# Kernel optimization log

Hardware: AMD Instinct MI355X
Metric: run time of the kernel (lower is better)

## Reference

```python
import jax, jax.numpy as jnp
import numpy as np

SQRT2 = 1.4142135623730951  # lrelu def_gain
LRELU_SLOPE = 0.2
EPS = 1e-8


def setup_inputs() -> dict:
    key = jax.random.key(0)
    k1, k2, k3, k4 = jax.random.split(key, 4)
    B, C_in, C_out, H, W, K, DLAT = 8, 512, 512, 32, 32, 3, 512
    x = jax.random.normal(k1, (B, C_in, H, W), dtype=jnp.float32)
    y = jax.random.normal(k2, (B, DLAT), dtype=jnp.float32)
    # init_std = 1.0 since use_wscale=True, lrmul=1
    weight = jax.random.normal(k3, (C_out, C_in, K, K), dtype=jnp.float32)
    mod_weight = jax.random.normal(k4, (C_in, DLAT), dtype=jnp.float32)
    bias = jnp.ones((C_in,), dtype=jnp.float32)
    return {"x": x, "y": y, "weight": weight, "mod_weight": mod_weight, "bias": bias}


def reference(x, y, weight, mod_weight, bias):
    B, C_in, H, W = x.shape
    C_out, _, K, _ = weight.shape
    dlat = mod_weight.shape[1]
    w_mul_mod = dlat ** (-0.5)  # EqualizedLinear wscale; conv w_mul is unused in forward
    # style: s = sqrt(2) * lrelu(y @ W_mod^T + b)
    s = y @ (mod_weight * w_mul_mod).T  # [B, C_in]
    s = jax.nn.leaky_relu(s + bias, LRELU_SLOPE) * SQRT2
    # modulate per-sample weights: [B, C_out, C_in, K, K]
    ww = weight[None] * s[:, None, :, None, None]
    # demodulate
    d = jax.lax.rsqrt(jnp.sum(ww * ww, axis=(2, 3, 4)) + EPS)  # [B, C_out]
    ww = ww * d[:, :, None, None, None]
    # fused grouped conv: groups = batch
    xg = x.reshape(1, B * C_in, H, W)
    wg = ww.reshape(B * C_out, C_in, K, K)
    out = jax.lax.conv_general_dilated(
        xg, wg, window_strides=(1, 1), padding="SAME",
        dimension_numbers=("NCHW", "OIHW", "NCHW"),
        feature_group_count=B)
    return out.reshape(B, C_out, H, W)
```

## Files before the change

### kernel.cpp

```cpp
#include <hip/hip_runtime.h>
#include <hip/hip_bf16.h>

typedef float f32x4 __attribute__((ext_vector_type(4)));
typedef short bf16x8 __attribute__((ext_vector_type(8)));

#define LRELU_SLOPE 0.2f
#define SQRT2F 1.4142135623730951f
#define MODSCALE 0.044194173824159216f

#define GLL(SRC, DST)                                                       \
  __builtin_amdgcn_global_load_lds(                                         \
      (const __attribute__((address_space(1))) unsigned int*)(SRC),         \
      (__attribute__((address_space(3))) unsigned int*)(DST), 16, 0, 0)

__global__ __launch_bounds__(256) void prep_kernel(const float* __restrict__ w,
                                                   const float* __restrict__ y,
                                                   const float* __restrict__ mw,
                                                   const float* __restrict__ bias,
                                                   __hip_bfloat16* __restrict__ wt2,
                                                   float* __restrict__ wsq,
                                                   float* __restrict__ s,
                                                   __hip_bfloat16* __restrict__ xsp) {
  const int bid = blockIdx.x;
  const int tid = threadIdx.x;
  if (bid < 1024) {
    int idx = bid * 256 + tid;
    int co = idx >> 9, ci = idx & 511;
    const float* p = w + (size_t)idx * 9;
    float v[9];
    float sq = 0.f;
#pragma unroll
    for (int t = 0; t < 9; ++t) {
      v[t] = p[t];
      sq += v[t] * v[t];
    }
    wsq[idx] = sq;
    int slabbase = ((ci >> 6) * 2 + ((ci >> 5) & 1)) * 16384 + co * 32 + (ci & 31);
#pragma unroll
    for (int t = 0; t < 9; ++t)
      wt2[t * 262144 + slabbase] = __float2bfloat16(v[t]);
  } else if (bid < 1152) {
    int l = tid & 63;
    int ci = (bid - 1024) * 4 + (tid >> 6);
    const float4* mwr = reinterpret_cast<const float4*>(mw + ci * 512);
    float4 m0 = mwr[2 * l], m1 = mwr[2 * l + 1];
    float acc[8];
#pragma unroll
    for (int b = 0; b < 8; ++b) {
      const float4* yr = reinterpret_cast<const float4*>(y + b * 512);
      float4 y0 = yr[2 * l], y1 = yr[2 * l + 1];
      acc[b] = m0.x * y0.x + m0.y * y0.y + m0.z * y0.z + m0.w * y0.w +
               m1.x * y1.x + m1.y * y1.y + m1.z * y1.z + m1.w * y1.w;
    }
#pragma unroll
    for (int off = 32; off > 0; off >>= 1) {
#pragma unroll
      for (int b = 0; b < 8; ++b) acc[b] += __shfl_xor(acc[b], off, 64);
    }
    if (l < 8) {
      float v = acc[l] * MODSCALE + bias[ci];
      v = v > 0.f ? v : LRELU_SLOPE * v;
      s[l * 512 + ci] = v * SQRT2F;
    }
  } else {
    int i = (bid - 1152) * 256 + tid;
    int b = i / 8448;
    int r = i - b * 8448;
    int pos = r >> 6;
    int cj = (r & 63) << 3;
    int hr, hc;
    if (pos < 34) { hr = 0; hc = pos; }
    else if (pos < 68) { hr = 33; hc = pos - 34; }
    else if (pos < 100) { hr = pos - 67; hc = 0; }
    else { hr = pos - 99; hc = 33; }
    unsigned off = (unsigned)((b * 34 + hr) * 34 + hc) * 512 + cj;
    int4 z = {0, 0, 0, 0};
    *reinterpret_cast<int4*>(xsp + off) = z;
  }
}

__global__ __launch_bounds__(256) void xsdem_kernel(const float* __restrict__ x,
                                                    const float* __restrict__ s,
                                                    const float* __restrict__ wsq,
                                                    __hip_bfloat16* __restrict__ xsp,
                                                    float* __restrict__ d) {
  const int bid = blockIdx.x;
  const int tid = threadIdx.x;
  if (bid < 2048) {
    int cc = bid & 7;
    int h = (bid >> 3) & 31;
    int b = bid >> 8;
    __shared__ __hip_bfloat16 tile[32][72];
    int cil = tid >> 2;
    int w0 = (tid & 3) * 8;
    int ci = cc * 64 + cil;
    const float* xp = x + (((size_t)(b * 512 + ci) * 32 + h) << 5) + w0;
    float sv = s[b * 512 + ci];
    float4 a0 = *reinterpret_cast<const float4*>(xp);
    float4 a1 = *reinterpret_cast<const float4*>(xp + 4);
    tile[w0 + 0][cil] = __float2bfloat16(a0.x * sv);
    tile[w0 + 1][cil] = __float2bfloat16(a0.y * sv);
    tile[w0 + 2][cil] = __float2bfloat16(a0.z * sv);
    tile[w0 + 3][cil] = __float2bfloat16(a0.w * sv);
    tile[w0 + 4][cil] = __float2bfloat16(a1.x * sv);
    tile[w0 + 5][cil] = __float2bfloat16(a1.y * sv);
    tile[w0 + 6][cil] = __float2bfloat16(a1.z * sv);
    tile[w0 + 7][cil] = __float2bfloat16(a1.w * sv);
    __syncthreads();
    int wloc = tid >> 3;
    int cj = (tid & 7) * 8;
    int4 v = *reinterpret_cast<const int4*>(&tile[wloc][cj]);
    unsigned off = (unsigned)((b * 34 + h + 1) * 34 + (wloc + 1)) * 512 + cc * 64 + cj;
    *reinterpret_cast<int4*>(xsp + off) = v;
  } else {
    int l = tid & 63;
    int co = (bid - 2048) * 4 + (tid >> 6);
    const float4* qr = reinterpret_cast<const float4*>(wsq + co * 512);
    float4 q0 = qr[2 * l], q1 = qr[2 * l + 1];
    float acc[8];
#pragma unroll
    for (int b = 0; b < 8; ++b) {
      const float4* sr = reinterpret_cast<const float4*>(s + b * 512);
      float4 s0 = sr[2 * l], s1 = sr[2 * l + 1];
      acc[b] = q0.x * s0.x * s0.x + q0.y * s0.y * s0.y + q0.z * s0.z * s0.z +
               q0.w * s0.w * s0.w + q1.x * s1.x * s1.x + q1.y * s1.y * s1.y +
               q1.z * s1.z * s1.z + q1.w * s1.w * s1.w;
    }
#pragma unroll
    for (int off = 32; off > 0; off >>= 1) {
#pragma unroll
      for (int b = 0; b < 8; ++b) acc[b] += __shfl_xor(acc[b], off, 64);
    }
    if (l < 8) d[l * 512 + co] = rsqrtf(acc[l] + 1e-8f);
  }
}

__global__ __launch_bounds__(512, 2) void conv_kernel(const __hip_bfloat16* __restrict__ xsp,
                                                      const __hip_bfloat16* __restrict__ wt2,
                                                      const float* __restrict__ dmod,
                                                      float* __restrict__ out) {
  __shared__ __hip_bfloat16 As_[2][224 * 64];
  __shared__ float red[16384];
  const int bid = blockIdx.x;
  const int xcd = bid & 7, slot0 = bid >> 3;
  const int bm = xcd * 8 + (slot0 >> 2);
  const int bn = slot0 & 3;
  const int tid = threadIdx.x;
  const int wv = tid >> 6;
  const int l = tid & 63;
  const int kg = wv >> 2;
  const int wr = (wv >> 1) & 1, wc = wv & 1;
  const int bb = bm >> 3;
  const int h0 = (bm & 7) << 2;

  unsigned ahoff[4];
  int adst[4];
#pragma unroll
  for (int j = 0; j < 4; ++j) {
    int rb = j < 3 ? j * 64 + wv * 8 : 192 + (wv & 3) * 8;
    int r = rb + (l >> 3);
    int rc = r > 203 ? 203 : r;
    int hr = rc / 34, hc = rc - hr * 34;
    ahoff[j] = (unsigned)((bb * 34 + h0 + hr) * 34 + hc) * 512 + (((l & 7) ^ (r & 7)) << 3);
    adst[j] = rb;
  }
  int pb[4];
#pragma unroll
  for (int m = 0; m < 4; ++m)
    pb[m] = ((wr << 1) + (m >> 1)) * 34 + ((m & 1) << 4) + (l & 15);

  const char* wtb = reinterpret_cast<const char*>(wt2);
  const unsigned nbase = (unsigned)(bn << 13) + (wc << 12) + ((l & 15) << 6) + ((l >> 4) << 4);

  f32x4 acc[4][4];
#pragma unroll
  for (int n = 0; n < 4; ++n)
#pragma unroll
    for (int m = 0; m < 4; ++m) acc[n][m] = (f32x4)0.f;

  bf16x8 fbk[2][4];

  auto stageA1 = [&](__hip_bfloat16* An, int j, int kn) {
    GLL(xsp + ahoff[j] + kn * 64, An + (adst[j] << 6));
  };
  auto loadB = [&](int bank, int t, int c) {
    const char* base = wtb + (size_t)(((t * 8 + c) * 2 + kg) << 15) + nbase;
#pragma unroll
    for (int n = 0; n < 4; ++n)
      fbk[bank][n] = *reinterpret_cast<const bf16x8*>(base + (n << 10));
  };
  auto doTap = [&](int bank, const __hip_bfloat16* Aq, int dh, int dw) {
    const int cb = (kg << 2) + (l >> 4);
    bf16x8 af[4];
#pragma unroll
    for (int m = 0; m < 4; ++m) {
      int p = pb[m] + dh * 34 + dw;
      af[m] = *reinterpret_cast<const bf16x8*>(Aq + p * 64 + ((cb ^ (p & 7)) << 3));
    }
    __builtin_amdgcn_s_setprio(1);
#pragma unroll
    for (int n = 0; n < 4; ++n)
#pragma unroll
      for (int m = 0; m < 4; ++m)
        acc[n][m] = __builtin_amdgcn_mfma_f32_16x16x32_bf16(fbk[bank][n], af[m], acc[n][m], 0, 0, 0);
    __builtin_amdgcn_s_setprio(0);
  };
  auto chunkBody = [&](int c, int P, bool stA, bool last) {
    const __hip_bfloat16* Aq = &As_[P][0];
    __hip_bfloat16* An = &As_[P ^ 1][0];
#pragma unroll
    for (int t = 0; t < 9; ++t) {
      if (!last || t < 8) loadB((P + t + 1) & 1, (t + 1) % 9, t < 8 ? c : c + 1);
      if (stA && t == 0) {
        stageA1(An, 0, c + 1); stageA1(An, 1, c + 1);
        stageA1(An, 2, c + 1); stageA1(An, 3, c + 1);
        __builtin_amdgcn_sched_barrier(0);
      }
      doTap((P + t) & 1, Aq, t / 3, t % 3);
    }
    if (!last) {
      asm volatile("s_waitcnt vmcnt(4)" ::: "memory");
      __builtin_amdgcn_s_barrier();
      __builtin_amdgcn_sched_barrier(0);
    }
  };

#pragma unroll
  for (int j = 0; j < 4; ++j) stageA1(&As_[0][0], j, 0);
  __builtin_amdgcn_sched_barrier(0);
  loadB(0, 0, 0);
  asm volatile("s_waitcnt vmcnt(4)" ::: "memory");
  __builtin_amdgcn_s_barrier();
  __builtin_amdgcn_sched_barrier(0);

#pragma unroll 1
  for (int kp = 0; kp < 3; ++kp) {
    chunkBody(2 * kp, 0, true, false);
    chunkBody(2 * kp + 1, 1, true, false);
  }
  chunkBody(6, 0, true, false);
  chunkBody(7, 1, false, true);

  __syncthreads();
  if (kg == 1) {
#pragma unroll
    for (int n = 0; n < 4; ++n)
#pragma unroll
      for (int m = 0; m < 4; ++m)
        *reinterpret_cast<f32x4*>(red + (n * 4 + m) * 1024 + (wv & 3) * 256 + l * 4) =
            acc[n][m];
  }
  __syncthreads();
  if (kg == 0) {
    const int pixbase = ((bm & 7) << 7) + (wr << 6) + (l & 15);
    const int cob = (bn << 7) + (wc << 6) + ((l >> 4) << 2);
    float* ob = out + ((size_t)bb << 19);
    const float* drow = dmod + bb * 512;
#pragma unroll
    for (int n = 0; n < 4; ++n) {
#pragma unroll
      for (int m = 0; m < 4; ++m)
        acc[n][m] += *reinterpret_cast<const f32x4*>(red + (n * 4 + m) * 1024 + wv * 256 + l * 4);
#pragma unroll
      for (int jj = 0; jj < 4; ++jj) {
        const int co = cob + (n << 4) + jj;
        const float dv = drow[co];
        float* orow = ob + ((unsigned)co << 10) + pixbase;
#pragma unroll
        for (int m = 0; m < 4; ++m) orow[m << 4] = acc[n][m][jj] * dv;
      }
    }
  }
}

extern "C" void kernel_launch(void* const* d_in, const int* in_sizes, int n_in,
                              void* d_out, int out_size, void* d_ws, size_t ws_size,
                              hipStream_t stream) {
  (void)in_sizes; (void)n_in; (void)out_size; (void)ws_size;
  const float* x = (const float*)d_in[0];
  const float* y = (const float*)d_in[1];
  const float* w = (const float*)d_in[2];
  const float* mw = (const float*)d_in[3];
  const float* bias = (const float*)d_in[4];
  float* out = (float*)d_out;

  char* ws = (char*)d_ws;
  float* s = (float*)(ws + 0);
  float* dmod = (float*)(ws + 16384);
  float* wsq = (float*)(ws + 32768);
  __hip_bfloat16* wt2 = (__hip_bfloat16*)(ws + 1081344);
  __hip_bfloat16* xsp = (__hip_bfloat16*)(ws + 5799936);

  prep_kernel<<<1416, 256, 0, stream>>>(w, y, mw, bias, wt2, wsq, s, xsp);
  xsdem_kernel<<<2176, 256, 0, stream>>>(x, s, wsq, xsp, dmod);
  conv_kernel<<<256, 512, 0, stream>>>(xsp, wt2, dmod, out);
}
```

Baseline: 59.87 us.

## Drop split-K across waves in conv; shrink N tile and double block count

The conv kernel no longer splits the K dimension across two wave groups with an LDS reduction. Each 256-thread block now computes a 64-channel output tile over the full 64-wide K slice, and the grid doubles to 512 blocks, mapped so each XCD handles one batch. This removes the shared-memory reduction buffer and its two barriers and frees LDS. In exchange, each block issues more A-staging loads (7 per thread instead of 4), and the activation tile is reused across fewer output channels, so more L2 traffic is needed.

```diff
diff --git a/kernel.cpp b/kernel.cpp
--- a/kernel.cpp
+++ b/kernel.cpp
@@ -135,29 +135,27 @@
   }
 }
 
-__global__ __launch_bounds__(512, 2) void conv_kernel(const __hip_bfloat16* __restrict__ xsp,
+__global__ __launch_bounds__(256, 2) void conv_kernel(const __hip_bfloat16* __restrict__ xsp,
                                                       const __hip_bfloat16* __restrict__ wt2,
                                                       const float* __restrict__ dmod,
                                                       float* __restrict__ out) {
   __shared__ __hip_bfloat16 As_[2][224 * 64];
-  __shared__ float red[16384];
   const int bid = blockIdx.x;
-  const int xcd = bid & 7, slot0 = bid >> 3;
-  const int bm = xcd * 8 + (slot0 >> 2);
-  const int bn = slot0 & 3;
+  const int xcd = bid & 7, slot = bid >> 3;
+  const int bmq = slot >> 3;
+  const int bn = slot & 7;
+  const int bb = xcd;
   const int tid = threadIdx.x;
   const int wv = tid >> 6;
   const int l = tid & 63;
-  const int kg = wv >> 2;
-  const int wr = (wv >> 1) & 1, wc = wv & 1;
-  const int bb = bm >> 3;
-  const int h0 = (bm & 7) << 2;
-
-  unsigned ahoff[4];
-  int adst[4];
-#pragma unroll
-  for (int j = 0; j < 4; ++j) {
-    int rb = j < 3 ? j * 64 + wv * 8 : 192 + (wv & 3) * 8;
+  const int wr = wv >> 1, wc = wv & 1;
+  const int h0 = bmq << 2;
+
+  unsigned ahoff[7];
+  int adst[7];
+#pragma unroll
+  for (int j = 0; j < 7; ++j) {
+    int rb = j * 32 + wv * 8;
     int r = rb + (l >> 3);
     int rc = r > 203 ? 203 : r;
     int hr = rc / 34, hc = rc - hr * 34;
@@ -170,40 +168,47 @@
     pb[m] = ((wr << 1) + (m >> 1)) * 34 + ((m & 1) << 4) + (l & 15);
 
   const char* wtb = reinterpret_cast<const char*>(wt2);
-  const unsigned nbase = (unsigned)(bn << 13) + (wc << 12) + ((l & 15) << 6) + ((l >> 4) << 4);
-
-  f32x4 acc[4][4];
-#pragma unroll
-  for (int n = 0; n < 4; ++n)
+  const unsigned nbase = (unsigned)(bn << 12) + (wc << 11) + ((l & 15) << 6) + ((l >> 4) << 4);
+
+  f32x4 acc[2][4];
+#pragma unroll
+  for (int n = 0; n < 2; ++n)
 #pragma unroll
     for (int m = 0; m < 4; ++m) acc[n][m] = (f32x4)0.f;
 
-  bf16x8 fbk[2][4];
+  bf16x8 fbk[2][2][2];
 
   auto stageA1 = [&](__hip_bfloat16* An, int j, int kn) {
     GLL(xsp + ahoff[j] + kn * 64, An + (adst[j] << 6));
   };
   auto loadB = [&](int bank, int t, int c) {
-    const char* base = wtb + (size_t)(((t * 8 + c) * 2 + kg) << 15) + nbase;
-#pragma unroll
-    for (int n = 0; n < 4; ++n)
-      fbk[bank][n] = *reinterpret_cast<const bf16x8*>(base + (n << 10));
+#pragma unroll
+    for (int kh = 0; kh < 2; ++kh) {
+      const char* base = wtb + (size_t)(((t * 8 + c) * 2 + kh) << 15) + nbase;
+#pragma unroll
+      for (int n = 0; n < 2; ++n)
+        fbk[bank][kh][n] = *reinterpret_cast<const bf16x8*>(base + (n << 10));
+    }
   };
   auto doTap = [&](int bank, const __hip_bfloat16* Aq, int dh, int dw) {
-    const int cb = (kg << 2) + (l >> 4);
-    bf16x8 af[4];
-#pragma unroll
-    for (int m = 0; m < 4; ++m) {
-      int p = pb[m] + dh * 34 + dw;
-      af[m] = *reinterpret_cast<const bf16x8*>(Aq + p * 64 + ((cb ^ (p & 7)) << 3));
-    }
-    __builtin_amdgcn_s_setprio(1);
-#pragma unroll
-    for (int n = 0; n < 4; ++n)
-#pragma unroll
-      for (int m = 0; m < 4; ++m)
-        acc[n][m] = __builtin_amdgcn_mfma_f32_16x16x32_bf16(fbk[bank][n], af[m], acc[n][m], 0, 0, 0);
-    __builtin_amdgcn_s_setprio(0);
+#pragma unroll
+    for (int kh = 0; kh < 2; ++kh) {
+      const int cb = (kh << 2) + (l >> 4);
+      bf16x8 af[4];
+#pragma unroll
+      for (int m = 0; m < 4; ++m) {
+        int p = pb[m] + dh * 34 + dw;
+        af[m] = *reinterpret_cast<const bf16x8*>(Aq + p * 64 + ((cb ^ (p & 7)) << 3));
+      }
+      __builtin_amdgcn_s_setprio(1);
+#pragma unroll
+      for (int n = 0; n < 2; ++n)
+#pragma unroll
+        for (int m = 0; m < 4; ++m)
+          acc[n][m] = __builtin_amdgcn_mfma_f32_16x16x32_bf16(fbk[bank][kh][n], af[m],
+                                                              acc[n][m], 0, 0, 0);
+      __builtin_amdgcn_s_setprio(0);
+    }
   };
   auto chunkBody = [&](int c, int P, bool stA, bool last) {
     const __hip_bfloat16* Aq = &As_[P][0];
@@ -212,8 +217,8 @@
     for (int t = 0; t < 9; ++t) {
       if (!last || t < 8) loadB((P + t + 1) & 1, (t + 1) % 9, t < 8 ? c : c + 1);
       if (stA && t == 0) {
-        stageA1(An, 0, c + 1); stageA1(An, 1, c + 1);
-        stageA1(An, 2, c + 1); stageA1(An, 3, c + 1);
+#pragma unroll
+        for (int j = 0; j < 7; ++j) stageA1(An, j, c + 1);
         __builtin_amdgcn_sched_barrier(0);
       }
       doTap((P + t) & 1, Aq, t / 3, t % 3);
@@ -226,7 +231,7 @@
   };
 
 #pragma unroll
-  for (int j = 0; j < 4; ++j) stageA1(&As_[0][0], j, 0);
+  for (int j = 0; j < 7; ++j) stageA1(&As_[0][0], j, 0);
   __builtin_amdgcn_sched_barrier(0);
   loadB(0, 0, 0);
   asm volatile("s_waitcnt vmcnt(4)" ::: "memory");
@@ -241,34 +246,19 @@
   chunkBody(6, 0, true, false);
   chunkBody(7, 1, false, true);
 
-  __syncthreads();
-  if (kg == 1) {
-#pragma unroll
-    for (int n = 0; n < 4; ++n)
-#pragma unroll
-      for (int m = 0; m < 4; ++m)
-        *reinterpret_cast<f32x4*>(red + (n * 4 + m) * 1024 + (wv & 3) * 256 + l * 4) =
-            acc[n][m];
-  }
-  __syncthreads();
-  if (kg == 0) {
-    const int pixbase = ((bm & 7) << 7) + (wr << 6) + (l & 15);
-    const int cob = (bn << 7) + (wc << 6) + ((l >> 4) << 2);
-    float* ob = out + ((size_t)bb << 19);
-    const float* drow = dmod + bb * 512;
-#pragma unroll
-    for (int n = 0; n < 4; ++n) {
-#pragma unroll
-      for (int m = 0; m < 4; ++m)
-        acc[n][m] += *reinterpret_cast<const f32x4*>(red + (n * 4 + m) * 1024 + wv * 256 + l * 4);
-#pragma unroll
-      for (int jj = 0; jj < 4; ++jj) {
-        const int co = cob + (n << 4) + jj;
-        const float dv = drow[co];
-        float* orow = ob + ((unsigned)co << 10) + pixbase;
-#pragma unroll
-        for (int m = 0; m < 4; ++m) orow[m << 4] = acc[n][m][jj] * dv;
-      }
+  const int pixbase = (bmq << 7) + (wr << 6) + (l & 15);
+  const int cob = (bn << 6) + (wc << 5) + ((l >> 4) << 2);
+  float* ob = out + ((size_t)bb << 19);
+  const float* drow = dmod + bb * 512;
+#pragma unroll
+  for (int n = 0; n < 2; ++n) {
+#pragma unroll
+    for (int jj = 0; jj < 4; ++jj) {
+      const int co = cob + (n << 4) + jj;
+      const float dv = drow[co];
+      float* orow = ob + ((unsigned)co << 10) + pixbase;
+#pragma unroll
+      for (int m = 0; m < 4; ++m) orow[m << 4] = acc[n][m][jj] * dv;
     }
   }
 }
@@ -293,5 +283,5 @@
 
   prep_kernel<<<1416, 256, 0, stream>>>(w, y, mw, bias, wt2, wsq, s, xsp);
   xsdem_kernel<<<2176, 256, 0, stream>>>(x, s, wsq, xsp, dmod);
-  conv_kernel<<<256, 512, 0, stream>>>(xsp, wt2, dmod, out);
-}
+  conv_kernel<<<512, 256, 0, stream>>>(xsp, wt2, dmod, out);
+}
```

New measurement: 59.17 us (median of 2 runs). Within noise of the previous version (-1.2%).
